# Optimization experiments

Measured on AMD Instinct MI355X. Metric: run time of the kernel, lower is better.

The kernel has to match this reference:

```python
import jax, jax.numpy as jnp
import numpy as np

NUM_FEATURES = 512
NUM_HID = 16
NUM_CLASSES = 40


def _glorot(key, shape):
    lim = float(np.sqrt(6.0 / (shape[0] + shape[1])))
    return jax.random.uniform(key, shape, jnp.float32, -lim, lim)


def setup_inputs() -> dict:
    key = jax.random.key(0)
    k1, k2, k3, k4 = jax.random.split(key, 4)
    N, E = 100000, 3200000
    x = jax.random.normal(k1, (N, NUM_FEATURES), jnp.float32)
    edge_index = jax.random.randint(k2, (2, E), 0, N, jnp.int64)
    W1 = _glorot(k3, (NUM_FEATURES, NUM_HID))
    b1 = jnp.zeros((NUM_HID,), jnp.float32)
    W2 = _glorot(k4, (NUM_HID, NUM_CLASSES))
    b2 = jnp.zeros((NUM_CLASSES,), jnp.float32)
    return {"x": x, "edge_index": edge_index, "num_nodes": N,
            "W1": W1, "b1": b1, "W2": W2, "b2": b2}


def gcn_conv(x, src, dst, norm, W, b, num_nodes):
    # linear transform first (PyG GCNConv), then normalized scatter-add
    h = x @ W                                    # [N, out]
    msg = h[src] * norm[:, None]                 # [E+N, out]
    agg = jax.ops.segment_sum(msg, dst, num_segments=num_nodes)
    return agg + b


def reference(x, edge_index, num_nodes, W1, b1, W2, b2):
    # add self-loops and compute symmetric normalization deg^-1/2 A_hat deg^-1/2
    loops = jnp.arange(num_nodes, dtype=edge_index.dtype)
    src = jnp.concatenate([edge_index[0], loops])
    dst = jnp.concatenate([edge_index[1], loops])
    ones = jnp.ones(src.shape, x.dtype)
    deg = jax.ops.segment_sum(ones, dst, num_segments=num_nodes)
    dinv = jnp.where(deg > 0, deg ** -0.5, 0.0)
    norm = dinv[src] * dinv[dst]

    h = jax.nn.relu(gcn_conv(x, src, dst, norm, W1, b1, num_nodes))
    # dropout omitted: inference mode (training=False)
    h = gcn_conv(h, src, dst, norm, W2, b2, num_nodes)
    out = jax.nn.softmax(h, axis=1)
    return (out, h)
```

## Files before the change

### kernel.cpp

```cpp
#include <hip/hip_runtime.h>
#include <math.h>

#define F 512
#define H 16
#define C 40
#define BW 128
#define BSH 7
#define NB_MAX 1024
#define CHUNK 4096
#define SEGS 8
#define SRC_BITS 17
#define SRC_MASK 0x1FFFF
#define SORT_CAP 8192

__global__ __launch_bounds__(256) void k_hist2(const int* __restrict__ dst,
                                               int* __restrict__ M, int E, int NB) {
    __shared__ int hist[NB_MAX];
    int c = blockIdx.x, t = threadIdx.x;
    for (int b = t; b < NB; b += 256) hist[b] = 0;
    __syncthreads();
    int i0 = c * CHUNK, end = min(i0 + CHUNK, E);
    for (int i = i0 + t; i < end; i += 256)
        atomicAdd(&hist[dst[i] >> BSH], 1);
    __syncthreads();
    for (int b = t; b < NB; b += 256) M[(size_t)c * NB + b] = hist[b];
}

__global__ __launch_bounds__(256) void k_csA(const int* __restrict__ M, int* __restrict__ P,
                                             int NB, int NCH, int SEGLEN) {
    int t = blockIdx.x * 256 + threadIdx.x;
    if (t >= SEGS * NB) return;
    int s = t / NB, b = t - s * NB;
    int c0 = s * SEGLEN, c1 = min(c0 + SEGLEN, NCH);
    int sum = 0;
    for (int c = c0; c < c1; c++) sum += M[(size_t)c * NB + b];
    P[s * NB + b] = sum;
}

__global__ __launch_bounds__(256) void k_csB(int* __restrict__ P, int* __restrict__ S, int NB) {
    int b = blockIdx.x * 256 + threadIdx.x;
    if (b >= NB) return;
    int run = 0;
    #pragma unroll
    for (int s = 0; s < SEGS; s++) {
        int v = P[s * NB + b];
        P[s * NB + b] = run;
        run += v;
    }
    S[b] = run;
}

__global__ void k_bscan(const int* __restrict__ S, int* __restrict__ brow,
                        int* __restrict__ rowptr, int NB, int N, int E) {
    __shared__ int sh[1024];
    int t = threadIdx.x;
    int v = (t < NB) ? S[t] : 0;
    sh[t] = v;
    __syncthreads();
    for (int off = 1; off < 1024; off <<= 1) {
        int add = (t >= off) ? sh[t - off] : 0;
        __syncthreads();
        sh[t] += add;
        __syncthreads();
    }
    if (t < NB) brow[t] = sh[t] - v;
    if (t == 0) { brow[NB] = E; rowptr[N] = E; }
}

__global__ __launch_bounds__(256) void k_csC(int* __restrict__ M, const int* __restrict__ P,
                                             const int* __restrict__ brow,
                                             int NB, int NCH, int SEGLEN) {
    int t = blockIdx.x * 256 + threadIdx.x;
    if (t >= SEGS * NB) return;
    int s = t / NB, b = t - s * NB;
    int c0 = s * SEGLEN, c1 = min(c0 + SEGLEN, NCH);
    int run = P[s * NB + b] + brow[b];
    for (int c = c0; c < c1; c++) {
        int v = M[(size_t)c * NB + b];
        M[(size_t)c * NB + b] = run;
        run += v;
    }
}

__global__ __launch_bounds__(256) void k_bscatter2(const int* __restrict__ src,
                                                   const int* __restrict__ dst,
                                                   const int* __restrict__ M,
                                                   int* __restrict__ ebuf, int E, int NB) {
    __shared__ int gbase[NB_MAX];
    __shared__ int hist[NB_MAX];
    int c = blockIdx.x, t = threadIdx.x;
    for (int b = t; b < NB; b += 256) {
        gbase[b] = M[(size_t)c * NB + b];
        hist[b] = 0;
    }
    __syncthreads();
    int i0 = c * CHUNK, end = min(i0 + CHUNK, E);
    for (int i = i0 + t; i < end; i += 256) {
        int d = dst[i], sv = src[i];
        int b = d >> BSH;
        int r = atomicAdd(&hist[b], 1);
        ebuf[gbase[b] + r] = ((d & (BW - 1)) << SRC_BITS) | sv;
    }
}

__global__ __launch_bounds__(256) void k_sortb(int* __restrict__ ebuf,
                                               const int* __restrict__ brow,
                                               int* __restrict__ rowptr,
                                               float* __restrict__ dinv, int N) {
    __shared__ int buf[SORT_CAP];
    __shared__ int hist[BW];
    __shared__ int off[BW];
    __shared__ int cur[BW];
    int b = blockIdx.x;
    int beg = brow[b], end = brow[b + 1];
    int len = end - beg;
    if (len > SORT_CAP) len = SORT_CAP;
    int tid = threadIdx.x;
    if (tid < BW) hist[tid] = 0;
    for (int i = tid; i < len; i += 256) buf[i] = ebuf[beg + i];
    __syncthreads();
    for (int i = tid; i < len; i += 256)
        atomicAdd(&hist[buf[i] >> SRC_BITS], 1);
    __syncthreads();
    if (tid < BW) off[tid] = hist[tid];
    __syncthreads();
    for (int d = 1; d < BW; d <<= 1) {
        int v = (tid < BW && tid >= d) ? off[tid - d] : 0;
        __syncthreads();
        if (tid < BW) off[tid] += v;
        __syncthreads();
    }
    if (tid < BW) {
        int excl = off[tid] - hist[tid];
        int n = b * BW + tid;
        if (n < N) {
            rowptr[n] = beg + excl;
            dinv[n] = rsqrtf((float)(hist[tid] + 1));
        }
        cur[tid] = excl;
    }
    __syncthreads();
    for (int i = tid; i < len; i += 256) {
        int w = buf[i];
        int r = atomicAdd(&cur[w >> SRC_BITS], 1);
        ebuf[beg + r] = w & SRC_MASK;
    }
}

#define KT 64
#define GST 68
__global__ __launch_bounds__(64) void k_gemm1(const float* __restrict__ x,
                                              const float* __restrict__ W1,
                                              const float* __restrict__ dinv,
                                              float* __restrict__ h0s, int N) {
    __shared__ float xs[64 * GST];
    int t = threadIdx.x;
    int n0 = blockIdx.x * 64;
    float acc[H];
    #pragma unroll
    for (int j = 0; j < H; j++) acc[j] = 0.f;
    for (int kt = 0; kt < F; kt += KT) {
        __syncthreads();
        #pragma unroll
        for (int p = 0; p < 16; p++) {
            int idx = t + (p << 6);
            int r = idx >> 4, c4 = idx & 15;
            int v = n0 + r; if (v >= N) v = N - 1;
            float4 val = *(const float4*)(x + (size_t)v * F + kt + (c4 << 2));
            *(float4*)&xs[r * GST + (c4 << 2)] = val;
        }
        __syncthreads();
        #pragma unroll
        for (int k4 = 0; k4 < 16; k4++) {
            float4 xv = *(const float4*)&xs[t * GST + (k4 << 2)];
            const float* w = W1 + (size_t)(kt + (k4 << 2)) * H;
            #pragma unroll
            for (int j = 0; j < H; j++) acc[j] = fmaf(xv.x, w[j], acc[j]);
            #pragma unroll
            for (int j = 0; j < H; j++) acc[j] = fmaf(xv.y, w[H + j], acc[j]);
            #pragma unroll
            for (int j = 0; j < H; j++) acc[j] = fmaf(xv.z, w[2 * H + j], acc[j]);
            #pragma unroll
            for (int j = 0; j < H; j++) acc[j] = fmaf(xv.w, w[3 * H + j], acc[j]);
        }
    }
    int v = n0 + t;
    if (v >= N) return;
    float dv = dinv[v];
    float4* o4 = (float4*)(h0s + (size_t)v * H);
    o4[0] = make_float4(acc[0] * dv, acc[1] * dv, acc[2] * dv, acc[3] * dv);
    o4[1] = make_float4(acc[4] * dv, acc[5] * dv, acc[6] * dv, acc[7] * dv);
    o4[2] = make_float4(acc[8] * dv, acc[9] * dv, acc[10] * dv, acc[11] * dv);
    o4[3] = make_float4(acc[12] * dv, acc[13] * dv, acc[14] * dv, acc[15] * dv);
}

__global__ __launch_bounds__(256) void k_agg1(const float* __restrict__ hs,
                                              const int* __restrict__ adj,
                                              const int* __restrict__ rowptr,
                                              const float* __restrict__ dinv,
                                              const float* __restrict__ b1,
                                              float* __restrict__ out, int N) {
    int t = blockIdx.x * 256 + threadIdx.x;
    int n = t >> 2, q = t & 3;
    if (n >= N) return;
    const float4* hs4 = (const float4*)hs;
    int beg = rowptr[n], end = rowptr[n + 1];
    float4 a = hs4[(size_t)n * 4 + q];
    float ax = a.x, ay = a.y, az = a.z, aw = a.w;
    int e = beg;
    for (; e + 3 < end; e += 4) {
        int s0 = adj[e], s1 = adj[e + 1], s2 = adj[e + 2], s3 = adj[e + 3];
        float4 v0 = hs4[(size_t)s0 * 4 + q];
        float4 v1 = hs4[(size_t)s1 * 4 + q];
        float4 v2 = hs4[(size_t)s2 * 4 + q];
        float4 v3 = hs4[(size_t)s3 * 4 + q];
        ax += (v0.x + v1.x) + (v2.x + v3.x);
        ay += (v0.y + v1.y) + (v2.y + v3.y);
        az += (v0.z + v1.z) + (v2.z + v3.z);
        aw += (v0.w + v1.w) + (v2.w + v3.w);
    }
    for (; e < end; e++) {
        int s = adj[e];
        float4 v = hs4[(size_t)s * 4 + q];
        ax += v.x; ay += v.y; az += v.z; aw += v.w;
    }
    float dv = dinv[n];
    float4 r;
    r.x = fmaxf(fmaf(dv, ax, b1[q * 4 + 0]), 0.f) * dv;
    r.y = fmaxf(fmaf(dv, ay, b1[q * 4 + 1]), 0.f) * dv;
    r.z = fmaxf(fmaf(dv, az, b1[q * 4 + 2]), 0.f) * dv;
    r.w = fmaxf(fmaf(dv, aw, b1[q * 4 + 3]), 0.f) * dv;
    ((float4*)out)[(size_t)n * 4 + q] = r;
}

__global__ __launch_bounds__(256) void k_agg2out(const float* __restrict__ hs,
                                                 const int* __restrict__ adj,
                                                 const int* __restrict__ rowptr,
                                                 const float* __restrict__ dinv,
                                                 const float* __restrict__ W2,
                                                 const float* __restrict__ b2,
                                                 float* __restrict__ dout, int N) {
    __shared__ float sg[64 * 16];
    __shared__ float w2s[H * C];
    __shared__ float b2s[C];
    int t = threadIdx.x;
    for (int i = t; i < H * C; i += 256) w2s[i] = W2[i];
    if (t < C) b2s[t] = b2[t];
    int nl = t >> 2, q = t & 3;
    int n = blockIdx.x * 64 + nl;
    bool valid = (n < N);
    int nn = valid ? n : N - 1;
    const float4* hs4 = (const float4*)hs;
    int beg = rowptr[nn], end = rowptr[nn + 1];
    float4 a = hs4[(size_t)nn * 4 + q];
    float ax = a.x, ay = a.y, az = a.z, aw = a.w;
    int e = beg;
    for (; e + 3 < end; e += 4) {
        int s0 = adj[e], s1 = adj[e + 1], s2 = adj[e + 2], s3 = adj[e + 3];
        float4 v0 = hs4[(size_t)s0 * 4 + q];
        float4 v1 = hs4[(size_t)s1 * 4 + q];
        float4 v2 = hs4[(size_t)s2 * 4 + q];
        float4 v3 = hs4[(size_t)s3 * 4 + q];
        ax += (v0.x + v1.x) + (v2.x + v3.x);
        ay += (v0.y + v1.y) + (v2.y + v3.y);
        az += (v0.z + v1.z) + (v2.z + v3.z);
        aw += (v0.w + v1.w) + (v2.w + v3.w);
    }
    for (; e < end; e++) {
        int s = adj[e];
        float4 v = hs4[(size_t)s * 4 + q];
        ax += v.x; ay += v.y; az += v.z; aw += v.w;
    }
    float dv = dinv[nn];
    *(float4*)&sg[nl * 16 + q * 4] = make_float4(dv * ax, dv * ay, dv * az, dv * aw);
    __syncthreads();
    float g16[16];
    #pragma unroll
    for (int k4 = 0; k4 < 4; k4++) {
        float4 gv = *(const float4*)&sg[nl * 16 + k4 * 4];
        g16[k4 * 4] = gv.x; g16[k4 * 4 + 1] = gv.y;
        g16[k4 * 4 + 2] = gv.z; g16[k4 * 4 + 3] = gv.w;
    }
    int j0 = q * 10;
    float h2[10];
    #pragma unroll
    for (int jj = 0; jj < 10; jj++) {
        float acc = b2s[j0 + jj];
        #pragma unroll
        for (int k = 0; k < H; k++) acc = fmaf(g16[k], w2s[k * C + j0 + jj], acc);
        h2[jj] = acc;
    }
    float m = h2[0];
    #pragma unroll
    for (int jj = 1; jj < 10; jj++) m = fmaxf(m, h2[jj]);
    m = fmaxf(m, __shfl_xor(m, 1, 64));
    m = fmaxf(m, __shfl_xor(m, 2, 64));
    float ex[10], s = 0.f;
    #pragma unroll
    for (int jj = 0; jj < 10; jj++) { ex[jj] = __expf(h2[jj] - m); s += ex[jj]; }
    s += __shfl_xor(s, 1, 64);
    s += __shfl_xor(s, 2, 64);
    float inv = 1.f / s;
    if (valid) {
        #pragma unroll
        for (int jj = 0; jj < 10; jj++)
            dout[(size_t)n * C + j0 + jj] = ex[jj] * inv;
        #pragma unroll
        for (int jj = 0; jj < 10; jj++)
            dout[(size_t)N * C + (size_t)n * C + j0 + jj] = h2[jj];
    }
}

extern "C" void kernel_launch(void* const* d_in, const int* in_sizes, int n_in,
                              void* d_out, int out_size, void* d_ws, size_t ws_size,
                              hipStream_t stream) {
    const float* x  = (const float*)d_in[0];
    const int*   ei = (const int*)d_in[1];
    const float* W1 = (const float*)d_in[3];
    const float* b1 = (const float*)d_in[4];
    const float* W2 = (const float*)d_in[5];
    const float* b2 = (const float*)d_in[6];
    float* out = (float*)d_out;

    int N = in_sizes[0] / F;
    int E = in_sizes[1] / 2;
    const int* src = ei;
    const int* dst = ei + E;
    int NB  = (N + BW - 1) / BW;
    int NCH = (E + CHUNK - 1) / CHUNK;
    int SEGLEN = (NCH + SEGS - 1) / SEGS;

    float* ws = (float*)d_ws;
    size_t o = 0;
    int* M      = (int*)(ws + o); o += (size_t)NCH * NB;
    int* P      = (int*)(ws + o); o += (size_t)SEGS * NB_MAX;
    int* S      = (int*)(ws + o); o += (size_t)NB_MAX;
    int* brow   = (int*)(ws + o); o += (size_t)NB_MAX + 4;
    int* rowptr = (int*)(ws + o); o += (size_t)N + 4;
    int* ebuf   = (int*)(ws + o); o += (size_t)E;
    float* dinv = ws + o;         o += (size_t)N;
    float* h0s  = ws + o;         o += (size_t)N * H;
    float* h1s  = ws + o;         o += (size_t)N * H;

    int ng  = (N + 63) / 64;
    int ncs = (SEGS * NB + 255) / 256;

    k_hist2    <<<NCH, 256, 0, stream>>>(dst, M, E, NB);
    k_csA      <<<ncs, 256, 0, stream>>>(M, P, NB, NCH, SEGLEN);
    k_csB      <<<(NB + 255) / 256, 256, 0, stream>>>(P, S, NB);
    k_bscan    <<<1, 1024, 0, stream>>>(S, brow, rowptr, NB, N, E);
    k_csC      <<<ncs, 256, 0, stream>>>(M, P, brow, NB, NCH, SEGLEN);
    k_bscatter2<<<NCH, 256, 0, stream>>>(src, dst, M, ebuf, E, NB);
    k_sortb    <<<NB, 256, 0, stream>>>(ebuf, brow, rowptr, dinv, N);
    k_gemm1    <<<ng, 64, 0, stream>>>(x, W1, dinv, h0s, N);
    k_agg1     <<<(N * 4 + 255) / 256, 256, 0, stream>>>(h0s, ebuf, rowptr, dinv, b1, h1s, N);
    k_agg2out  <<<ng, 256, 0, stream>>>(h1s, ebuf, rowptr, dinv, W2, b2, out, N);
}
```

Before: 601.5 us.

## Stage bucket scatter in LDS, fuse scan kernels, unroll gathers, coalesce output stores

Fuses the per-bucket segment scan into the single-block bucket scan kernel, removing one launch and the S buffer. The bucket scatter now builds a local counting sort in shared memory and writes edges to global memory in bucket-contiguous order, aiming for better-coalesced writes. Both aggregation kernels get an 8-way unrolled neighbor gather to keep more loads in flight. The final kernel stages softmax and logits rows in shared memory and writes them as coalesced float4 stores. In exchange, the scatter kernel uses much more shared memory per block, which can lower occupancy.

```diff
diff --git a/kernel.cpp b/kernel.cpp
--- a/kernel.cpp
+++ b/kernel.cpp
@@ -37,25 +37,20 @@
     P[s * NB + b] = sum;
 }
 
-__global__ __launch_bounds__(256) void k_csB(int* __restrict__ P, int* __restrict__ S, int NB) {
-    int b = blockIdx.x * 256 + threadIdx.x;
-    if (b >= NB) return;
-    int run = 0;
-    #pragma unroll
-    for (int s = 0; s < SEGS; s++) {
-        int v = P[s * NB + b];
-        P[s * NB + b] = run;
-        run += v;
-    }
-    S[b] = run;
-}
-
-__global__ void k_bscan(const int* __restrict__ S, int* __restrict__ brow,
-                        int* __restrict__ rowptr, int NB, int N, int E) {
+__global__ void k_csBscan(int* __restrict__ P, int* __restrict__ brow,
+                          int* __restrict__ rowptr, int NB, int N, int E) {
     __shared__ int sh[1024];
     int t = threadIdx.x;
-    int v = (t < NB) ? S[t] : 0;
-    sh[t] = v;
+    int run = 0;
+    if (t < NB) {
+        #pragma unroll
+        for (int s = 0; s < SEGS; s++) {
+            int v = P[s * NB + t];
+            P[s * NB + t] = run;
+            run += v;
+        }
+    }
+    sh[t] = run;
     __syncthreads();
     for (int off = 1; off < 1024; off <<= 1) {
         int add = (t >= off) ? sh[t - off] : 0;
@@ -63,7 +58,7 @@
         sh[t] += add;
         __syncthreads();
     }
-    if (t < NB) brow[t] = sh[t] - v;
+    if (t < NB) brow[t] = sh[t] - run;
     if (t == 0) { brow[NB] = E; rowptr[N] = E; }
 }
 
@@ -82,25 +77,58 @@
     }
 }
 
-__global__ __launch_bounds__(256) void k_bscatter2(const int* __restrict__ src,
+__global__ __launch_bounds__(256) void k_bscatter3(const int* __restrict__ src,
                                                    const int* __restrict__ dst,
                                                    const int* __restrict__ M,
                                                    int* __restrict__ ebuf, int E, int NB) {
     __shared__ int gbase[NB_MAX];
-    __shared__ int hist[NB_MAX];
+    __shared__ int pos[NB_MAX];
+    __shared__ int cur[NB_MAX];
+    __shared__ int tsum[256];
+    __shared__ int paddr[CHUNK];
+    __shared__ int pdata[CHUNK];
     int c = blockIdx.x, t = threadIdx.x;
     for (int b = t; b < NB; b += 256) {
         gbase[b] = M[(size_t)c * NB + b];
-        hist[b] = 0;
+        cur[b] = 0;
     }
     __syncthreads();
     int i0 = c * CHUNK, end = min(i0 + CHUNK, E);
+    for (int i = i0 + t; i < end; i += 256)
+        atomicAdd(&cur[dst[i] >> BSH], 1);
+    __syncthreads();
+    int b0 = t * 4;
+    int v0 = (b0 + 0 < NB) ? cur[b0 + 0] : 0;
+    int v1 = (b0 + 1 < NB) ? cur[b0 + 1] : 0;
+    int v2 = (b0 + 2 < NB) ? cur[b0 + 2] : 0;
+    int v3 = (b0 + 3 < NB) ? cur[b0 + 3] : 0;
+    int loc1 = v0, loc2 = v0 + v1, loc3 = v0 + v1 + v2;
+    int s = loc3 + v3;
+    tsum[t] = s;
+    __syncthreads();
+    for (int off = 1; off < 256; off <<= 1) {
+        int v = (t >= off) ? tsum[t - off] : 0;
+        __syncthreads();
+        tsum[t] += v;
+        __syncthreads();
+    }
+    int excl = tsum[t] - s;
+    if (b0 + 0 < NB) { int p = excl;        pos[b0 + 0] = p; cur[b0 + 0] = p; }
+    if (b0 + 1 < NB) { int p = excl + loc1; pos[b0 + 1] = p; cur[b0 + 1] = p; }
+    if (b0 + 2 < NB) { int p = excl + loc2; pos[b0 + 2] = p; cur[b0 + 2] = p; }
+    if (b0 + 3 < NB) { int p = excl + loc3; pos[b0 + 3] = p; cur[b0 + 3] = p; }
+    __syncthreads();
     for (int i = i0 + t; i < end; i += 256) {
         int d = dst[i], sv = src[i];
         int b = d >> BSH;
-        int r = atomicAdd(&hist[b], 1);
-        ebuf[gbase[b] + r] = ((d & (BW - 1)) << SRC_BITS) | sv;
-    }
+        int r = atomicAdd(&cur[b], 1);
+        paddr[r] = gbase[b] + (r - pos[b]);
+        pdata[r] = ((d & (BW - 1)) << SRC_BITS) | sv;
+    }
+    __syncthreads();
+    int n = end - i0;
+    for (int i = t; i < n; i += 256)
+        ebuf[paddr[i]] = pdata[i];
 }
 
 __global__ __launch_bounds__(256) void k_sortb(int* __restrict__ ebuf,
@@ -208,6 +236,22 @@
     float4 a = hs4[(size_t)n * 4 + q];
     float ax = a.x, ay = a.y, az = a.z, aw = a.w;
     int e = beg;
+    for (; e + 7 < end; e += 8) {
+        int s0 = adj[e], s1 = adj[e + 1], s2 = adj[e + 2], s3 = adj[e + 3];
+        int s4 = adj[e + 4], s5 = adj[e + 5], s6 = adj[e + 6], s7 = adj[e + 7];
+        float4 v0 = hs4[(size_t)s0 * 4 + q];
+        float4 v1 = hs4[(size_t)s1 * 4 + q];
+        float4 v2 = hs4[(size_t)s2 * 4 + q];
+        float4 v3 = hs4[(size_t)s3 * 4 + q];
+        float4 v4 = hs4[(size_t)s4 * 4 + q];
+        float4 v5 = hs4[(size_t)s5 * 4 + q];
+        float4 v6 = hs4[(size_t)s6 * 4 + q];
+        float4 v7 = hs4[(size_t)s7 * 4 + q];
+        ax += ((v0.x + v1.x) + (v2.x + v3.x)) + ((v4.x + v5.x) + (v6.x + v7.x));
+        ay += ((v0.y + v1.y) + (v2.y + v3.y)) + ((v4.y + v5.y) + (v6.y + v7.y));
+        az += ((v0.z + v1.z) + (v2.z + v3.z)) + ((v4.z + v5.z) + (v6.z + v7.z));
+        aw += ((v0.w + v1.w) + (v2.w + v3.w)) + ((v4.w + v5.w) + (v6.w + v7.w));
+    }
     for (; e + 3 < end; e += 4) {
         int s0 = adj[e], s1 = adj[e + 1], s2 = adj[e + 2], s3 = adj[e + 3];
         float4 v0 = hs4[(size_t)s0 * 4 + q];
@@ -243,11 +287,13 @@
     __shared__ float sg[64 * 16];
     __shared__ float w2s[H * C];
     __shared__ float b2s[C];
+    __shared__ float so[64 * 40];
     int t = threadIdx.x;
     for (int i = t; i < H * C; i += 256) w2s[i] = W2[i];
     if (t < C) b2s[t] = b2[t];
     int nl = t >> 2, q = t & 3;
-    int n = blockIdx.x * 64 + nl;
+    int n0 = blockIdx.x * 64;
+    int n = n0 + nl;
     bool valid = (n < N);
     int nn = valid ? n : N - 1;
     const float4* hs4 = (const float4*)hs;
@@ -255,6 +301,22 @@
     float4 a = hs4[(size_t)nn * 4 + q];
     float ax = a.x, ay = a.y, az = a.z, aw = a.w;
     int e = beg;
+    for (; e + 7 < end; e += 8) {
+        int s0 = adj[e], s1 = adj[e + 1], s2 = adj[e + 2], s3 = adj[e + 3];
+        int s4 = adj[e + 4], s5 = adj[e + 5], s6 = adj[e + 6], s7 = adj[e + 7];
+        float4 v0 = hs4[(size_t)s0 * 4 + q];
+        float4 v1 = hs4[(size_t)s1 * 4 + q];
+        float4 v2 = hs4[(size_t)s2 * 4 + q];
+        float4 v3 = hs4[(size_t)s3 * 4 + q];
+        float4 v4 = hs4[(size_t)s4 * 4 + q];
+        float4 v5 = hs4[(size_t)s5 * 4 + q];
+        float4 v6 = hs4[(size_t)s6 * 4 + q];
+        float4 v7 = hs4[(size_t)s7 * 4 + q];
+        ax += ((v0.x + v1.x) + (v2.x + v3.x)) + ((v4.x + v5.x) + (v6.x + v7.x));
+        ay += ((v0.y + v1.y) + (v2.y + v3.y)) + ((v4.y + v5.y) + (v6.y + v7.y));
+        az += ((v0.z + v1.z) + (v2.z + v3.z)) + ((v4.z + v5.z) + (v6.z + v7.z));
+        aw += ((v0.w + v1.w) + (v2.w + v3.w)) + ((v4.w + v5.w) + (v6.w + v7.w));
+    }
     for (; e + 3 < end; e += 4) {
         int s0 = adj[e], s1 = adj[e + 1], s2 = adj[e + 2], s3 = adj[e + 3];
         float4 v0 = hs4[(size_t)s0 * 4 + q];
@@ -295,19 +357,30 @@
     for (int jj = 1; jj < 10; jj++) m = fmaxf(m, h2[jj]);
     m = fmaxf(m, __shfl_xor(m, 1, 64));
     m = fmaxf(m, __shfl_xor(m, 2, 64));
-    float ex[10], s = 0.f;
-    #pragma unroll
-    for (int jj = 0; jj < 10; jj++) { ex[jj] = __expf(h2[jj] - m); s += ex[jj]; }
-    s += __shfl_xor(s, 1, 64);
-    s += __shfl_xor(s, 2, 64);
-    float inv = 1.f / s;
-    if (valid) {
-        #pragma unroll
-        for (int jj = 0; jj < 10; jj++)
-            dout[(size_t)n * C + j0 + jj] = ex[jj] * inv;
-        #pragma unroll
-        for (int jj = 0; jj < 10; jj++)
-            dout[(size_t)N * C + (size_t)n * C + j0 + jj] = h2[jj];
+    float ex[10], ssum = 0.f;
+    #pragma unroll
+    for (int jj = 0; jj < 10; jj++) { ex[jj] = __expf(h2[jj] - m); ssum += ex[jj]; }
+    ssum += __shfl_xor(ssum, 1, 64);
+    ssum += __shfl_xor(ssum, 2, 64);
+    float inv = 1.f / ssum;
+    int rows = min(64, N - n0);
+    int tot = rows * 10;
+    #pragma unroll
+    for (int jj = 0; jj < 10; jj++) so[nl * 40 + j0 + jj] = ex[jj] * inv;
+    __syncthreads();
+    {
+        const float4* sp4 = (const float4*)so;
+        float4* o4 = (float4*)(dout + (size_t)n0 * C);
+        for (int i = t; i < tot; i += 256) o4[i] = sp4[i];
+    }
+    __syncthreads();
+    #pragma unroll
+    for (int jj = 0; jj < 10; jj++) so[nl * 40 + j0 + jj] = h2[jj];
+    __syncthreads();
+    {
+        const float4* sp4 = (const float4*)so;
+        float4* o4 = (float4*)(dout + (size_t)N * C + (size_t)n0 * C);
+        for (int i = t; i < tot; i += 256) o4[i] = sp4[i];
     }
 }
 
@@ -334,7 +407,6 @@
     size_t o = 0;
     int* M      = (int*)(ws + o); o += (size_t)NCH * NB;
     int* P      = (int*)(ws + o); o += (size_t)SEGS * NB_MAX;
-    int* S      = (int*)(ws + o); o += (size_t)NB_MAX;
     int* brow   = (int*)(ws + o); o += (size_t)NB_MAX + 4;
     int* rowptr = (int*)(ws + o); o += (size_t)N + 4;
     int* ebuf   = (int*)(ws + o); o += (size_t)E;
@@ -347,10 +419,9 @@
 
     k_hist2    <<<NCH, 256, 0, stream>>>(dst, M, E, NB);
     k_csA      <<<ncs, 256, 0, stream>>>(M, P, NB, NCH, SEGLEN);
-    k_csB      <<<(NB + 255) / 256, 256, 0, stream>>>(P, S, NB);
-    k_bscan    <<<1, 1024, 0, stream>>>(S, brow, rowptr, NB, N, E);
+    k_csBscan  <<<1, 1024, 0, stream>>>(P, brow, rowptr, NB, N, E);
     k_csC      <<<ncs, 256, 0, stream>>>(M, P, brow, NB, NCH, SEGLEN);
-    k_bscatter2<<<NCH, 256, 0, stream>>>(src, dst, M, ebuf, E, NB);
+    k_bscatter3<<<NCH, 256, 0, stream>>>(src, dst, M, ebuf, E, NB);
     k_sortb    <<<NB, 256, 0, stream>>>(ebuf, brow, rowptr, dinv, N);
     k_gemm1    <<<ng, 64, 0, stream>>>(x, W1, dinv, h0s, N);
     k_agg1     <<<(N * 4 + 255) / 256, 256, 0, stream>>>(h0s, ebuf, rowptr, dinv, b1, h1s, N);
```

Measured after the change: 554.8 us. 1.08x faster.
